# Optimization experiments

Hardware: AMD Instinct MI355X
Metric: run time of the kernel (lower is better)

The kernel has to match this reference:

```python
import jax, jax.numpy as jnp
import numpy as np
import math


def setup_inputs() -> dict:
    key = jax.random.key(0)
    k0, k1, k2, k3, k4 = jax.random.split(key, 5)
    in_f, out_f, nb = 512, 512, 8
    B, S = 4, 2048
    x = jax.random.normal(k0, (B, S, in_f), dtype=jnp.float32)
    # RBF params (frozen in original: basis_trainable=False)
    fan_in = in_f  # fan_in of rbf.weight.T which is (num_basis, in_features)
    bound = 1.0 / math.sqrt(fan_in)
    rbf_weight = jax.random.uniform(k1, (in_f, nb), dtype=jnp.float32,
                                    minval=-math.sqrt(3.0) * 0.33 / math.sqrt(fan_in),
                                    maxval=math.sqrt(3.0) * 0.33 / math.sqrt(fan_in))
    rbf_centers = jnp.tile(jnp.linspace(-bound, bound, nb, dtype=jnp.float32)[None, :], (in_f, 1))
    # KAN spline weight (in, nb, out); fan_in for init is in_f*nb
    fan2 = in_f * nb
    wb = math.sqrt(3.0) * 0.33 / math.sqrt(fan2)
    weight = jax.random.uniform(k2, (in_f, nb, out_f), dtype=jnp.float32, minval=-wb, maxval=wb)
    bias = jax.random.uniform(k3, (out_f,), dtype=jnp.float32,
                              minval=-1.0 / math.sqrt(fan2), maxval=1.0 / math.sqrt(fan2))
    scale_base = jax.random.uniform(k4, (in_f, out_f), dtype=jnp.float32, minval=-0.1, maxval=0.1)
    return {"x": x, "rbf_weight": rbf_weight, "rbf_centers": rbf_centers,
            "weight": weight, "bias": bias, "scale_base": scale_base}


def reference(x, rbf_weight, rbf_centers, weight, bias, scale_base):
    in_f = x.shape[-1]
    nb = rbf_weight.shape[1]
    beta = (nb / math.log2(nb)) ** 2  # get_rbf_width(2/nb, log2(nb))
    batch_shape = x.shape[:-1]
    xf = x.reshape(-1, in_f)  # (N, in)
    # RBF basis expansion: (N, in, nb)
    z = xf[:, :, None] * rbf_weight[None, :, :] - rbf_centers[None, :, :]
    phi = jnp.exp(-beta * (z * z))
    # spline contraction + base path, expressed as efficient contractions
    y = jnp.einsum('nib,ibo->no', phi, weight)
    y = y + bias + jnp.cos(xf) @ scale_base
    return y.reshape(*batch_shape, weight.shape[-1])
```

## Files before the change

### kernel.cpp

```cpp
#include <hip/hip_runtime.h>
#include <hip/hip_bf16.h>

typedef __attribute__((ext_vector_type(8))) short short8;
typedef __attribute__((ext_vector_type(4))) float f32x4;

#define IN_F 512
#define OUT_F 512
#define BM 128
#define BN 128
#define BK 64
#define THREADS 512
#define PHI_STEPS 64
#define NSTEPS 72
#define NT 4
#define KSPLIT 2
#define SPL (NSTEPS / KSPLIT)
#define IMG_CHUNKS 1024
#define IMG_SHORTS (IMG_CHUNKS * 8)
#define PART_ELEMS (8192 * OUT_F)

__device__ __forceinline__ short f2bf(float f) {
  __hip_bfloat16 h = __float2bfloat16(f);
  return __builtin_bit_cast(short, h);
}

__device__ __forceinline__ void glds16(const void* g, void* l) {
  __builtin_amdgcn_global_load_lds(
      (const __attribute__((address_space(1))) unsigned int*)g,
      (__attribute__((address_space(3))) unsigned int*)l, 16, 0, 0);
}

__device__ __forceinline__ float bsrc(const float* __restrict__ w,
                                      const float* __restrict__ sb,
                                      int k, int col) {
  return (k < IN_F * 8) ? w[(size_t)k * OUT_F + col]
                        : sb[(size_t)(k - IN_F * 8) * OUT_F + col];
}

__global__ void __launch_bounds__(256) prep_b(const float* __restrict__ w,
                                              const float* __restrict__ sb,
                                              short* __restrict__ img) {
  const int D = blockIdx.x * 256 + threadIdx.x;
  const int ci = D & (IMG_CHUNKS - 1);
  const int im = D >> 10;
  const int s = im % NSTEPS;
  const int nt = im / NSTEPS;
  const int n = ci >> 3, slot = ci & 7;
  const int oct = slot ^ (n & 7);
  const int col = nt * BN + n;
  short8 v;
#pragma unroll
  for (int j = 0; j < 8; ++j) v[j] = f2bf(bsrc(w, sb, s * 64 + oct * 8 + j, col));
  *(short8*)&img[(size_t)D * 8] = v;
}

__global__ void __launch_bounds__(256) reduce2(const float* __restrict__ part,
                                               const float* __restrict__ bias,
                                               float* __restrict__ out) {
  const int n4 = PART_ELEMS / 4;
  const float4* p0 = (const float4*)part;
  const float4* p1 = (const float4*)(part + PART_ELEMS);
  const float4* b4 = (const float4*)bias;
  float4* o4 = (float4*)out;
  for (int i = blockIdx.x * 256 + threadIdx.x; i < n4; i += gridDim.x * 256) {
    const float4 a = p0[i], b = p1[i], bb = b4[i & (OUT_F / 4 - 1)];
    float4 r;
    r.x = a.x + b.x + bb.x; r.y = a.y + b.y + bb.y;
    r.z = a.z + b.z + bb.z; r.w = a.w + b.w + bb.w;
    o4[i] = r;
  }
}

template <int KS, bool PREB>
__global__ void __launch_bounds__(THREADS, 4) kan_split(
    const float* __restrict__ x, const float* __restrict__ rw,
    const float* __restrict__ rc, const float* __restrict__ w,
    const float* __restrict__ bias, const float* __restrict__ sb,
    const short* __restrict__ bimg, float* __restrict__ dst) {
  __shared__ __align__(16) short A_lds[BM * BK];
  __shared__ __align__(16) short B_lds[BN * BK];

  const int t = threadIdx.x, lane = t & 63, wid = t >> 6;
  const int wm = wid >> 2;
  const int wn = wid & 3;
  const int l15 = lane & 15, kb = lane >> 4;

  const int m0 = blockIdx.x * BM;
  const int nt = blockIdx.y, n0 = nt * BN;
  const int ks = blockIdx.z;
  const int s0 = ks * SPL;

  f32x4 acc[4][2];
#pragma unroll
  for (int i = 0; i < 4; ++i)
#pragma unroll
    for (int j = 0; j < 2; ++j) acc[i][j] = (f32x4){0.f, 0.f, 0.f, 0.f};

  const int a_il = t & 7;
  const int a_m = t >> 3;
  const int b_n = t & 127;
  const int b_o = t >> 7;

  const float c2 = -10.259164f;

  for (int si = 0; si < SPL; ++si) {
    const int s = s0 + si;
    __syncthreads();

    if (PREB) {
      const short* src = bimg + ((size_t)(nt * NSTEPS + s) * IMG_CHUNKS + t) * 8;
      glds16(src, &B_lds[wid * 512]);
      glds16(src + IMG_SHORTS / 2, &B_lds[IMG_SHORTS / 2 + wid * 512]);
    }

    if (s < PHI_STEPS) {
      const int feat = s * 8 + a_il;
      const float4 rw0 = *(const float4*)(rw + feat * 8);
      const float4 rw1 = *(const float4*)(rw + feat * 8 + 4);
      const float4 rc0 = *(const float4*)(rc + feat * 8);
      const float4 rc1 = *(const float4*)(rc + feat * 8 + 4);
      const float rwv[8] = {rw0.x, rw0.y, rw0.z, rw0.w, rw1.x, rw1.y, rw1.z, rw1.w};
      const float rcv[8] = {rc0.x, rc0.y, rc0.z, rc0.w, rc1.x, rc1.y, rc1.z, rc1.w};
#pragma unroll
      for (int iter = 0; iter < 2; ++iter) {
        const int m = a_m + iter * 64;
        const float xv = x[(size_t)(m0 + m) * IN_F + feat];
        short8 av;
#pragma unroll
        for (int b = 0; b < 8; ++b) {
          const float z = fmaf(xv, rwv[b], -rcv[b]);
          av[b] = f2bf(exp2f(c2 * z * z));
        }
        *(short8*)&A_lds[m * BK + (a_il ^ (m & 7)) * 8] = av;
      }
    } else {
      const int f0 = (s - PHI_STEPS) * 64 + a_il * 8;
#pragma unroll
      for (int iter = 0; iter < 2; ++iter) {
        const int m = a_m + iter * 64;
        const float4 xa = *(const float4*)(x + (size_t)(m0 + m) * IN_F + f0);
        const float4 xb = *(const float4*)(x + (size_t)(m0 + m) * IN_F + f0 + 4);
        short8 av;
        av[0] = f2bf(__cosf(xa.x)); av[1] = f2bf(__cosf(xa.y));
        av[2] = f2bf(__cosf(xa.z)); av[3] = f2bf(__cosf(xa.w));
        av[4] = f2bf(__cosf(xb.x)); av[5] = f2bf(__cosf(xb.y));
        av[6] = f2bf(__cosf(xb.z)); av[7] = f2bf(__cosf(xb.w));
        *(short8*)&A_lds[m * BK + (a_il ^ (m & 7)) * 8] = av;
      }
    }

    if (!PREB) {
      const float* Bs = (s < PHI_STEPS) ? (w + (size_t)s * 64 * OUT_F)
                                        : (sb + (size_t)(s - PHI_STEPS) * 64 * OUT_F);
      const float* p0 = Bs + (b_o * 8) * OUT_F + n0 + b_n;
      const float* p1 = Bs + ((b_o + 4) * 8) * OUT_F + n0 + b_n;
      short8 v0, v1;
#pragma unroll
      for (int j = 0; j < 8; ++j) { v0[j] = f2bf(p0[j * OUT_F]); v1[j] = f2bf(p1[j * OUT_F]); }
      *(short8*)&B_lds[b_n * BK + (b_o ^ (b_n & 7)) * 8] = v0;
      *(short8*)&B_lds[b_n * BK + ((b_o + 4) ^ (b_n & 7)) * 8] = v1;
    }

    __syncthreads();

#pragma unroll
    for (int kk = 0; kk < 2; ++kk) {
      short8 af[4], bv[2];
      const int slotk = kk * 4 + kb;
#pragma unroll
      for (int mi = 0; mi < 4; ++mi) {
        const int r = wm * 64 + mi * 16 + l15;
        af[mi] = *(const short8*)&A_lds[r * BK + (slotk ^ (r & 7)) * 8];
      }
#pragma unroll
      for (int ni = 0; ni < 2; ++ni) {
        const int n = wn * 32 + ni * 16 + l15;
        bv[ni] = *(const short8*)&B_lds[n * BK + (slotk ^ (n & 7)) * 8];
      }
#pragma unroll
      for (int mi = 0; mi < 4; ++mi)
#pragma unroll
        for (int ni = 0; ni < 2; ++ni)
          acc[mi][ni] = __builtin_amdgcn_mfma_f32_16x16x32_bf16(
              af[mi], bv[ni], acc[mi][ni], 0, 0, 0);
    }
  }

#pragma unroll
  for (int ni = 0; ni < 2; ++ni) {
    const int col = n0 + wn * 32 + ni * 16 + l15;
    const float bb = (KS == 1) ? bias[col] : 0.f;
#pragma unroll
    for (int mi = 0; mi < 4; ++mi) {
      const int rb = m0 + wm * 64 + mi * 16 + kb * 4;
#pragma unroll
      for (int r4 = 0; r4 < 4; ++r4) {
        const size_t idx = (size_t)(rb + r4) * OUT_F + col;
        if (KS == 1) dst[idx] = acc[mi][ni][r4] + bb;
        else         dst[(size_t)ks * PART_ELEMS + idx] = acc[mi][ni][r4];
      }
    }
  }
}

extern "C" void kernel_launch(void* const* d_in, const int* in_sizes, int n_in,
                              void* d_out, int out_size, void* d_ws, size_t ws_size,
                              hipStream_t stream) {
  const float* x    = (const float*)d_in[0];
  const float* rw   = (const float*)d_in[1];
  const float* rc   = (const float*)d_in[2];
  const float* w    = (const float*)d_in[3];
  const float* bias = (const float*)d_in[4];
  const float* sb   = (const float*)d_in[5];
  float* out = (float*)d_out;

  const int nrows = in_sizes[0] / IN_F;

  const size_t img_bytes  = (size_t)NT * NSTEPS * IMG_SHORTS * sizeof(short);
  const size_t part_bytes = (size_t)KSPLIT * PART_ELEMS * sizeof(float);
  const int img_chunks_total = NT * NSTEPS * IMG_CHUNKS;

  if (ws_size >= img_bytes + part_bytes) {
    short* img = (short*)d_ws;
    float* part = (float*)((char*)d_ws + img_bytes);
    prep_b<<<img_chunks_total / 256, 256, 0, stream>>>(w, sb, img);
    dim3 grid(nrows / BM, NT, KSPLIT);
    kan_split<KSPLIT, true><<<grid, THREADS, 0, stream>>>(x, rw, rc, w, bias, sb, img, part);
    reduce2<<<2048, 256, 0, stream>>>(part, bias, out);
  } else if (ws_size >= img_bytes) {
    short* img = (short*)d_ws;
    prep_b<<<img_chunks_total / 256, 256, 0, stream>>>(w, sb, img);
    dim3 grid(nrows / BM, NT, 1);
    kan_split<1, true><<<grid, THREADS, 0, stream>>>(x, rw, rc, w, bias, sb, img, out);
  } else {
    dim3 grid(nrows / BM, NT, 1);
    kan_split<1, false><<<grid, THREADS, 0, stream>>>(x, rw, rc, w, bias, sb, nullptr, out);
  }
}
```

Baseline: 98.96 us.

## Use full-width 64x512 tiles with double-buffered LDS and single-partial reduction

Each block now owns a 64-row by 512-column output tile, so the RBF/cos basis for each row block is computed once instead of once per N tile. LDS is double-buffered so the next step's basis generation and B loads overlap the current step's MFMAs. The K split now writes the first half plus bias straight to the output, and the reduction kernel only adds the second partial into it. The cost is larger LDS use, lower occupancy (launch bounds 2), fewer blocks in the grid, and a read-modify-write of the output in the reduce pass.

```diff
diff --git a/kernel.cpp b/kernel.cpp
--- a/kernel.cpp
+++ b/kernel.cpp
@@ -6,17 +6,17 @@
 
 #define IN_F 512
 #define OUT_F 512
-#define BM 128
-#define BN 128
+#define BM 64
+#define BN 512
 #define BK 64
 #define THREADS 512
 #define PHI_STEPS 64
 #define NSTEPS 72
-#define NT 4
 #define KSPLIT 2
 #define SPL (NSTEPS / KSPLIT)
-#define IMG_CHUNKS 1024
-#define IMG_SHORTS (IMG_CHUNKS * 8)
+#define IMG_CHUNKS 4096
+#define A_SH (BM * BK)
+#define B_SH (BN * BK)
 #define PART_ELEMS (8192 * OUT_F)
 
 __device__ __forceinline__ short f2bf(float f) {
@@ -42,162 +42,145 @@
                                               short* __restrict__ img) {
   const int D = blockIdx.x * 256 + threadIdx.x;
   const int ci = D & (IMG_CHUNKS - 1);
-  const int im = D >> 10;
-  const int s = im % NSTEPS;
-  const int nt = im / NSTEPS;
+  const int s = D >> 12;
   const int n = ci >> 3, slot = ci & 7;
   const int oct = slot ^ (n & 7);
-  const int col = nt * BN + n;
   short8 v;
 #pragma unroll
-  for (int j = 0; j < 8; ++j) v[j] = f2bf(bsrc(w, sb, s * 64 + oct * 8 + j, col));
+  for (int j = 0; j < 8; ++j) v[j] = f2bf(bsrc(w, sb, s * 64 + oct * 8 + j, n));
   *(short8*)&img[(size_t)D * 8] = v;
 }
 
-__global__ void __launch_bounds__(256) reduce2(const float* __restrict__ part,
-                                               const float* __restrict__ bias,
-                                               float* __restrict__ out) {
+__global__ void __launch_bounds__(256) reduce_add(const float* __restrict__ part,
+                                                  float* __restrict__ out) {
   const int n4 = PART_ELEMS / 4;
-  const float4* p0 = (const float4*)part;
-  const float4* p1 = (const float4*)(part + PART_ELEMS);
-  const float4* b4 = (const float4*)bias;
+  const float4* p4 = (const float4*)part;
   float4* o4 = (float4*)out;
   for (int i = blockIdx.x * 256 + threadIdx.x; i < n4; i += gridDim.x * 256) {
-    const float4 a = p0[i], b = p1[i], bb = b4[i & (OUT_F / 4 - 1)];
-    float4 r;
-    r.x = a.x + b.x + bb.x; r.y = a.y + b.y + bb.y;
-    r.z = a.z + b.z + bb.z; r.w = a.w + b.w + bb.w;
-    o4[i] = r;
+    float4 a = o4[i];
+    const float4 b = p4[i];
+    a.x += b.x; a.y += b.y; a.z += b.z; a.w += b.w;
+    o4[i] = a;
   }
 }
 
 template <int KS, bool PREB>
-__global__ void __launch_bounds__(THREADS, 4) kan_split(
+__global__ void __launch_bounds__(THREADS, 2) kan_main(
     const float* __restrict__ x, const float* __restrict__ rw,
     const float* __restrict__ rc, const float* __restrict__ w,
     const float* __restrict__ bias, const float* __restrict__ sb,
-    const short* __restrict__ bimg, float* __restrict__ dst) {
-  __shared__ __align__(16) short A_lds[BM * BK];
-  __shared__ __align__(16) short B_lds[BN * BK];
+    const short* __restrict__ bimg, float* __restrict__ out,
+    float* __restrict__ part) {
+  __shared__ __align__(16) short A_lds[2][A_SH];
+  __shared__ __align__(16) short B_lds[2][B_SH];
 
   const int t = threadIdx.x, lane = t & 63, wid = t >> 6;
-  const int wm = wid >> 2;
-  const int wn = wid & 3;
   const int l15 = lane & 15, kb = lane >> 4;
-
   const int m0 = blockIdx.x * BM;
-  const int nt = blockIdx.y, n0 = nt * BN;
-  const int ks = blockIdx.z;
+  const int ks = (KS == 2) ? blockIdx.y : 0;
   const int s0 = ks * SPL;
-
-  f32x4 acc[4][2];
-#pragma unroll
-  for (int i = 0; i < 4; ++i)
-#pragma unroll
-    for (int j = 0; j < 2; ++j) acc[i][j] = (f32x4){0.f, 0.f, 0.f, 0.f};
 
   const int a_il = t & 7;
   const int a_m = t >> 3;
-  const int b_n = t & 127;
-  const int b_o = t >> 7;
-
-  const float c2 = -10.259164f;
-
-  for (int si = 0; si < SPL; ++si) {
-    const int s = s0 + si;
-    __syncthreads();
-
+  const float c2 = -10.2591705f;
+
+  f32x4 acc[4][4];
+#pragma unroll
+  for (int i = 0; i < 4; ++i)
+#pragma unroll
+    for (int j = 0; j < 4; ++j) acc[i][j] = (f32x4){0.f, 0.f, 0.f, 0.f};
+
+  auto stage = [&](int s, short* __restrict__ Ad, short* __restrict__ Bd) {
     if (PREB) {
-      const short* src = bimg + ((size_t)(nt * NSTEPS + s) * IMG_CHUNKS + t) * 8;
-      glds16(src, &B_lds[wid * 512]);
-      glds16(src + IMG_SHORTS / 2, &B_lds[IMG_SHORTS / 2 + wid * 512]);
-    }
-
+      const short* src = bimg + ((size_t)s * IMG_CHUNKS + t) * 8;
+#pragma unroll
+      for (int c = 0; c < 8; ++c)
+        glds16(src + (size_t)c * 512 * 8, Bd + c * 4096 + wid * 512);
+    } else {
+#pragma unroll
+      for (int c = 0; c < 8; ++c) {
+        const int ci = c * 512 + t;
+        const int n = ci >> 3, slot = ci & 7, oct = slot ^ (n & 7);
+        short8 v;
+#pragma unroll
+        for (int j = 0; j < 8; ++j) v[j] = f2bf(bsrc(w, sb, s * 64 + oct * 8 + j, n));
+        *(short8*)&Bd[ci * 8] = v;
+      }
+    }
+    short8 av;
     if (s < PHI_STEPS) {
       const int feat = s * 8 + a_il;
-      const float4 rw0 = *(const float4*)(rw + feat * 8);
-      const float4 rw1 = *(const float4*)(rw + feat * 8 + 4);
-      const float4 rc0 = *(const float4*)(rc + feat * 8);
-      const float4 rc1 = *(const float4*)(rc + feat * 8 + 4);
-      const float rwv[8] = {rw0.x, rw0.y, rw0.z, rw0.w, rw1.x, rw1.y, rw1.z, rw1.w};
-      const float rcv[8] = {rc0.x, rc0.y, rc0.z, rc0.w, rc1.x, rc1.y, rc1.z, rc1.w};
-#pragma unroll
-      for (int iter = 0; iter < 2; ++iter) {
-        const int m = a_m + iter * 64;
-        const float xv = x[(size_t)(m0 + m) * IN_F + feat];
-        short8 av;
-#pragma unroll
-        for (int b = 0; b < 8; ++b) {
-          const float z = fmaf(xv, rwv[b], -rcv[b]);
-          av[b] = f2bf(exp2f(c2 * z * z));
-        }
-        *(short8*)&A_lds[m * BK + (a_il ^ (m & 7)) * 8] = av;
+      const float xv = x[(size_t)(m0 + a_m) * IN_F + feat];
+      const float4 r0 = *(const float4*)(rw + feat * 8);
+      const float4 r1 = *(const float4*)(rw + feat * 8 + 4);
+      const float4 q0 = *(const float4*)(rc + feat * 8);
+      const float4 q1 = *(const float4*)(rc + feat * 8 + 4);
+      const float rwv[8] = {r0.x, r0.y, r0.z, r0.w, r1.x, r1.y, r1.z, r1.w};
+      const float rcv[8] = {q0.x, q0.y, q0.z, q0.w, q1.x, q1.y, q1.z, q1.w};
+#pragma unroll
+      for (int b = 0; b < 8; ++b) {
+        const float z = fmaf(xv, rwv[b], -rcv[b]);
+        av[b] = f2bf(exp2f(c2 * z * z));
       }
     } else {
-      const int f0 = (s - PHI_STEPS) * 64 + a_il * 8;
-#pragma unroll
-      for (int iter = 0; iter < 2; ++iter) {
-        const int m = a_m + iter * 64;
-        const float4 xa = *(const float4*)(x + (size_t)(m0 + m) * IN_F + f0);
-        const float4 xb = *(const float4*)(x + (size_t)(m0 + m) * IN_F + f0 + 4);
-        short8 av;
-        av[0] = f2bf(__cosf(xa.x)); av[1] = f2bf(__cosf(xa.y));
-        av[2] = f2bf(__cosf(xa.z)); av[3] = f2bf(__cosf(xa.w));
-        av[4] = f2bf(__cosf(xb.x)); av[5] = f2bf(__cosf(xb.y));
-        av[6] = f2bf(__cosf(xb.z)); av[7] = f2bf(__cosf(xb.w));
-        *(short8*)&A_lds[m * BK + (a_il ^ (m & 7)) * 8] = av;
-      }
-    }
-
-    if (!PREB) {
-      const float* Bs = (s < PHI_STEPS) ? (w + (size_t)s * 64 * OUT_F)
-                                        : (sb + (size_t)(s - PHI_STEPS) * 64 * OUT_F);
-      const float* p0 = Bs + (b_o * 8) * OUT_F + n0 + b_n;
-      const float* p1 = Bs + ((b_o + 4) * 8) * OUT_F + n0 + b_n;
-      short8 v0, v1;
-#pragma unroll
-      for (int j = 0; j < 8; ++j) { v0[j] = f2bf(p0[j * OUT_F]); v1[j] = f2bf(p1[j * OUT_F]); }
-      *(short8*)&B_lds[b_n * BK + (b_o ^ (b_n & 7)) * 8] = v0;
-      *(short8*)&B_lds[b_n * BK + ((b_o + 4) ^ (b_n & 7)) * 8] = v1;
-    }
-
+      const float* xp = x + (size_t)(m0 + a_m) * IN_F + (s - PHI_STEPS) * 64 + a_il * 8;
+      const float4 xa = *(const float4*)xp;
+      const float4 xb = *(const float4*)(xp + 4);
+      av[0] = f2bf(__cosf(xa.x)); av[1] = f2bf(__cosf(xa.y));
+      av[2] = f2bf(__cosf(xa.z)); av[3] = f2bf(__cosf(xa.w));
+      av[4] = f2bf(__cosf(xb.x)); av[5] = f2bf(__cosf(xb.y));
+      av[6] = f2bf(__cosf(xb.z)); av[7] = f2bf(__cosf(xb.w));
+    }
+    Ad[a_m * BK + (a_il ^ (a_m & 7)) * 8 + 0] = av[0];
+    *(short8*)&Ad[a_m * BK + (a_il ^ (a_m & 7)) * 8] = av;
+  };
+
+  auto mfma_step = [&](const short* __restrict__ Ab, const short* __restrict__ Bb) {
+#pragma unroll
+    for (int kk = 0; kk < 2; ++kk) {
+      const int sk = kk * 4 + kb;
+      short8 af[4], bf[4];
+#pragma unroll
+      for (int mi = 0; mi < 4; ++mi) {
+        const int r = mi * 16 + l15;
+        af[mi] = *(const short8*)&Ab[r * BK + (sk ^ (r & 7)) * 8];
+      }
+#pragma unroll
+      for (int ni = 0; ni < 4; ++ni) {
+        const int n = wid * 64 + ni * 16 + l15;
+        bf[ni] = *(const short8*)&Bb[n * BK + (sk ^ (n & 7)) * 8];
+      }
+#pragma unroll
+      for (int mi = 0; mi < 4; ++mi)
+#pragma unroll
+        for (int ni = 0; ni < 4; ++ni)
+          acc[mi][ni] = __builtin_amdgcn_mfma_f32_16x16x32_bf16(
+              af[mi], bf[ni], acc[mi][ni], 0, 0, 0);
+    }
+  };
+
+  stage(s0, A_lds[0], B_lds[0]);
+  __syncthreads();
+#pragma unroll 2
+  for (int si = 0; si < SPL; ++si) {
+    const int cur = si & 1;
+    if (si + 1 < SPL) stage(s0 + si + 1, A_lds[cur ^ 1], B_lds[cur ^ 1]);
+    mfma_step(A_lds[cur], B_lds[cur]);
     __syncthreads();
-
-#pragma unroll
-    for (int kk = 0; kk < 2; ++kk) {
-      short8 af[4], bv[2];
-      const int slotk = kk * 4 + kb;
-#pragma unroll
-      for (int mi = 0; mi < 4; ++mi) {
-        const int r = wm * 64 + mi * 16 + l15;
-        af[mi] = *(const short8*)&A_lds[r * BK + (slotk ^ (r & 7)) * 8];
-      }
-#pragma unroll
-      for (int ni = 0; ni < 2; ++ni) {
-        const int n = wn * 32 + ni * 16 + l15;
-        bv[ni] = *(const short8*)&B_lds[n * BK + (slotk ^ (n & 7)) * 8];
-      }
-#pragma unroll
-      for (int mi = 0; mi < 4; ++mi)
-#pragma unroll
-        for (int ni = 0; ni < 2; ++ni)
-          acc[mi][ni] = __builtin_amdgcn_mfma_f32_16x16x32_bf16(
-              af[mi], bv[ni], acc[mi][ni], 0, 0, 0);
-    }
-  }
-
-#pragma unroll
-  for (int ni = 0; ni < 2; ++ni) {
-    const int col = n0 + wn * 32 + ni * 16 + l15;
-    const float bb = (KS == 1) ? bias[col] : 0.f;
+  }
+
+#pragma unroll
+  for (int ni = 0; ni < 4; ++ni) {
+    const int col = wid * 64 + ni * 16 + l15;
+    const float bb = (KS == 1 || ks == 0) ? bias[col] : 0.f;
 #pragma unroll
     for (int mi = 0; mi < 4; ++mi) {
-      const int rb = m0 + wm * 64 + mi * 16 + kb * 4;
+      const int rb = m0 + mi * 16 + kb * 4;
 #pragma unroll
       for (int r4 = 0; r4 < 4; ++r4) {
         const size_t idx = (size_t)(rb + r4) * OUT_F + col;
-        if (KS == 1) dst[idx] = acc[mi][ni][r4] + bb;
-        else         dst[(size_t)ks * PART_ELEMS + idx] = acc[mi][ni][r4];
+        if (KS == 1 || ks == 0) out[idx] = acc[mi][ni][r4] + bb;
+        else                    part[idx] = acc[mi][ni][r4];
       }
     }
   }
@@ -216,24 +199,27 @@
 
   const int nrows = in_sizes[0] / IN_F;
 
-  const size_t img_bytes  = (size_t)NT * NSTEPS * IMG_SHORTS * sizeof(short);
-  const size_t part_bytes = (size_t)KSPLIT * PART_ELEMS * sizeof(float);
-  const int img_chunks_total = NT * NSTEPS * IMG_CHUNKS;
+  const size_t img_bytes  = (size_t)NSTEPS * IMG_CHUNKS * 16;
+  const size_t part_bytes = (size_t)PART_ELEMS * sizeof(float);
+  const int img_chunks_total = NSTEPS * IMG_CHUNKS;
 
   if (ws_size >= img_bytes + part_bytes) {
     short* img = (short*)d_ws;
     float* part = (float*)((char*)d_ws + img_bytes);
     prep_b<<<img_chunks_total / 256, 256, 0, stream>>>(w, sb, img);
-    dim3 grid(nrows / BM, NT, KSPLIT);
-    kan_split<KSPLIT, true><<<grid, THREADS, 0, stream>>>(x, rw, rc, w, bias, sb, img, part);
-    reduce2<<<2048, 256, 0, stream>>>(part, bias, out);
-  } else if (ws_size >= img_bytes) {
-    short* img = (short*)d_ws;
-    prep_b<<<img_chunks_total / 256, 256, 0, stream>>>(w, sb, img);
-    dim3 grid(nrows / BM, NT, 1);
-    kan_split<1, true><<<grid, THREADS, 0, stream>>>(x, rw, rc, w, bias, sb, img, out);
+    dim3 grid(nrows / BM, KSPLIT);
+    kan_main<KSPLIT, true><<<grid, THREADS, 0, stream>>>(x, rw, rc, w, bias, sb,
+                                                         img, out, part);
+    reduce_add<<<2048, 256, 0, stream>>>(part, out);
+  } else if (ws_size >= part_bytes) {
+    float* part = (float*)d_ws;
+    dim3 grid(nrows / BM, KSPLIT);
+    kan_main<KSPLIT, false><<<grid, THREADS, 0, stream>>>(x, rw, rc, w, bias, sb,
+                                                          nullptr, out, part);
+    reduce_add<<<2048, 256, 0, stream>>>(part, out);
   } else {
-    dim3 grid(nrows / BM, NT, 1);
-    kan_split<1, false><<<grid, THREADS, 0, stream>>>(x, rw, rc, w, bias, sb, nullptr, out);
-  }
-}
+    dim3 grid(nrows / BM, 1);
+    kan_main<1, false><<<grid, THREADS, 0, stream>>>(x, rw, rc, w, bias, sb,
+                                                     nullptr, out, nullptr);
+  }
+}
```

Measured after the change: 85.15 us. 14.0% less time.
